# Kernel tuning notes

Measured on AMD Instinct MI355X. Metric: run time of the kernel, lower is better.

## Reference

```python
import jax, jax.numpy as jnp
import numpy as np

N_NODES = 100000
N_EDGES = 1600000
IN_CH, HID_CH, OUT_CH = 128, 64, 64


def setup_inputs() -> dict:
    key = jax.random.key(0)
    k1, k2, k3, k4 = jax.random.split(key, 4)
    x = jax.random.normal(k1, (N_NODES, IN_CH), dtype=jnp.float32)
    edge_index = jax.random.randint(k2, (2, N_EDGES), 0, N_NODES, dtype=jnp.int64)
    # Glorot-style init for GCNConv linear weights; zero bias (PyG default)
    W1 = jax.random.normal(k3, (IN_CH, HID_CH), dtype=jnp.float32) * (1.0 / np.sqrt(IN_CH))
    b1 = jnp.zeros((HID_CH,), dtype=jnp.float32)
    W2 = jax.random.normal(k4, (HID_CH, OUT_CH), dtype=jnp.float32) * (1.0 / np.sqrt(HID_CH))
    b2 = jnp.zeros((OUT_CH,), dtype=jnp.float32)
    return {"x": x, "edge_index": edge_index, "W1": W1, "b1": b1, "W2": W2, "b2": b2}


def gcn_conv(x, row, col, W, b):
    # PyG GCNConv: linear transform, then sym-normalized scatter-add aggregation
    h = x @ W  # [N, out]
    ones = jnp.ones(col.shape, dtype=h.dtype)
    deg = jax.ops.segment_sum(ones, col, num_segments=N_NODES)  # in-degree incl. self-loops
    dinv = jnp.where(deg > 0, jax.lax.rsqrt(deg), 0.0)
    norm = dinv[row] * dinv[col]  # [E+N]
    msg = h[row] * norm[:, None]  # gather + scale, [E+N, out]
    out = jax.ops.segment_sum(msg, col, num_segments=N_NODES)  # scatter-add
    return out + b


def reference(x, edge_index, W1, b1, W2, b2):
    # add self-loops once (same edge set for both layers)
    loops = jnp.arange(N_NODES, dtype=edge_index.dtype)
    row = jnp.concatenate([edge_index[0], loops])
    col = jnp.concatenate([edge_index[1], loops])
    h = jax.nn.relu(gcn_conv(x, row, col, W1, b1))
    return gcn_conv(h, row, col, W2, b2)
```

## Files before the change

kernel.cpp:

```cpp
#include <hip/hip_runtime.h>


#define BKT_SH 7
#define BKT_CAP 4096
#define CHUNK 6144
#define BM 128
#define BK 32

__device__ __forceinline__ unsigned short f2bf(float f) {
    unsigned u = __builtin_bit_cast(unsigned, f);
    u = (u + 0x7FFF + ((u >> 16) & 1)) >> 16;
    return (unsigned short)u;
}
__device__ __forceinline__ float bflo(unsigned u) {
    return __builtin_bit_cast(float, u << 16);
}
__device__ __forceinline__ float bfhi(unsigned u) {
    return __builtin_bit_cast(float, u & 0xFFFF0000u);
}

__global__ __launch_bounds__(256) void k_zero_i(int* __restrict__ p, int n) {
    int i = blockIdx.x * 256 + threadIdx.x;
    if (i < n) p[i] = 0;
}

__global__ __launch_bounds__(256) void k_bin(const int* __restrict__ row,
                                             const int* __restrict__ col,
                                             int* __restrict__ cursor,
                                             unsigned* __restrict__ bentries,
                                             int E) {
    __shared__ unsigned sorted[CHUNK];
    __shared__ unsigned short bof[CHUNK];
    __shared__ int hist[1024];
    __shared__ int ex0[1024];
    __shared__ int cur[1024];
    __shared__ int gbase[1024];
    __shared__ int tsum[256];
    int b = blockIdx.x, t = threadIdx.x;
    int s0 = b * CHUNK;
    int cnt = E - s0; if (cnt > CHUNK) cnt = CHUNK;

    for (int i = t; i < 1024; i += 256) hist[i] = 0;
    __syncthreads();
    for (int i = t; i < cnt; i += 256)
        atomicAdd(&hist[col[s0 + i] >> BKT_SH], 1);
    __syncthreads();
    {
        int b0 = hist[4 * t], b1 = hist[4 * t + 1], b2 = hist[4 * t + 2], b3 = hist[4 * t + 3];
        int tot = b0 + b1 + b2 + b3;
        tsum[t] = tot;
        __syncthreads();
#pragma unroll
        for (int d = 1; d < 256; d <<= 1) {
            int x = (t >= d) ? tsum[t - d] : 0;
            __syncthreads();
            tsum[t] += (t >= d) ? x : 0;
            __syncthreads();
        }
        int ex = tsum[t] - tot;
        ex0[4 * t] = ex;
        ex0[4 * t + 1] = ex + b0;
        ex0[4 * t + 2] = ex + b0 + b1;
        ex0[4 * t + 3] = ex + b0 + b1 + b2;
        cur[4 * t] = ex0[4 * t];
        cur[4 * t + 1] = ex0[4 * t + 1];
        cur[4 * t + 2] = ex0[4 * t + 2];
        cur[4 * t + 3] = ex0[4 * t + 3];
    }
    __syncthreads();
    for (int i = t; i < 1024; i += 256)
        if (hist[i] > 0) gbase[i] = i * BKT_CAP + atomicAdd(&cursor[i], hist[i]);
    for (int i = t; i < cnt; i += 256) {
        int c = col[s0 + i], r = row[s0 + i];
        int bkt = c >> BKT_SH;
        int p = atomicAdd(&cur[bkt], 1);
        sorted[p] = ((unsigned)(c & ((1 << BKT_SH) - 1)) << 17) | (unsigned)r;
        bof[p] = (unsigned short)bkt;
    }
    __syncthreads();
    for (int i = t; i < cnt; i += 256) {
        int bkt = bof[i];
        int pos = gbase[bkt] + (i - ex0[bkt]);
        if (pos < (bkt + 1) * BKT_CAP) bentries[pos] = sorted[i];
    }
}

__global__ __launch_bounds__(256) void k_bucket_sort(
    unsigned* __restrict__ bentries, const int* __restrict__ cursor,
    int* __restrict__ start, int* __restrict__ cntarr,
    float* __restrict__ dinv, int N) {
    __shared__ int hist[128];
    __shared__ int incl[128];
    __shared__ int cur[128];
    __shared__ int rows[BKT_CAP];
    int b = blockIdx.x, t = threadIdx.x;
    int base = b * BKT_CAP;
    int cnt = cursor[b];
    if (cnt > BKT_CAP) cnt = BKT_CAP;

    if (t < 128) hist[t] = 0;
    __syncthreads();
    for (int i = t; i < cnt; i += 256)
        atomicAdd(&hist[bentries[base + i] >> 17], 1);
    __syncthreads();
    if (t < 128) incl[t] = hist[t];
    __syncthreads();
#pragma unroll
    for (int d = 1; d < 128; d <<= 1) {
        int x = (t < 128 && t >= d) ? incl[t - d] : 0;
        __syncthreads();
        if (t < 128 && t >= d) incl[t] += x;
        __syncthreads();
    }
    if (t < 128) {
        int ex = incl[t] - hist[t];
        int node = (b << BKT_SH) + t;
        if (node < N) {
            start[node] = base + ex;
            cntarr[node] = hist[t];
            dinv[node] = rsqrtf((float)hist[t] + 1.0f);
        }
        cur[t] = ex;
    }
    __syncthreads();
    for (int i = t; i < cnt; i += 256) {
        unsigned en = bentries[base + i];
        int p = atomicAdd(&cur[en >> 17], 1);
        rows[p] = (int)(en & 0x1FFFF);
    }
    __syncthreads();
    for (int i = t; i < cnt; i += 256) bentries[base + i] = (unsigned)rows[i];
}

__global__ __launch_bounds__(256) void k_gemm_f32in(
    const float* __restrict__ X, const float* __restrict__ W,
    const float* __restrict__ dinv, unsigned short* __restrict__ outb,
    int N, int K) {
    __shared__ float Xs[BK][BM + 4];
    __shared__ float Ws[BK][64];
    int t = threadIdx.x;
    int bm = blockIdx.x * BM;
    int tm = t >> 4, tn = t & 15;

    float acc[8][4];
#pragma unroll
    for (int i = 0; i < 8; ++i)
#pragma unroll
        for (int j = 0; j < 4; ++j) acc[i][j] = 0.f;

    for (int kb = 0; kb < K; kb += BK) {
#pragma unroll
        for (int it = 0; it < 4; ++it) {
            int r = (t >> 3) + 32 * it;
            int grow = bm + r;
            int k4 = t & 7;
            float4 v = make_float4(0.f, 0.f, 0.f, 0.f);
            if (grow < N) v = *(const float4*)(X + (size_t)grow * K + kb + k4 * 4);
            Xs[k4 * 4 + 0][r] = v.x;
            Xs[k4 * 4 + 1][r] = v.y;
            Xs[k4 * 4 + 2][r] = v.z;
            Xs[k4 * 4 + 3][r] = v.w;
        }
#pragma unroll
        for (int it = 0; it < 2; ++it) {
            int idx = t + 256 * it;
            ((float4*)Ws)[idx] = ((const float4*)(W + (size_t)kb * 64))[idx];
        }
        __syncthreads();
#pragma unroll
        for (int k = 0; k < BK; ++k) {
            float4 xa = *(const float4*)&Xs[k][tm * 8];
            float4 xb = *(const float4*)&Xs[k][tm * 8 + 4];
            float4 w = *(const float4*)&Ws[k][tn * 4];
            float xs[8] = {xa.x, xa.y, xa.z, xa.w, xb.x, xb.y, xb.z, xb.w};
#pragma unroll
            for (int i = 0; i < 8; ++i) {
                acc[i][0] = fmaf(xs[i], w.x, acc[i][0]);
                acc[i][1] = fmaf(xs[i], w.y, acc[i][1]);
                acc[i][2] = fmaf(xs[i], w.z, acc[i][2]);
                acc[i][3] = fmaf(xs[i], w.w, acc[i][3]);
            }
        }
        __syncthreads();
    }
#pragma unroll
    for (int i = 0; i < 8; ++i) {
        int grow = bm + tm * 8 + i;
        if (grow < N) {
            float s = dinv[grow];
            ushort4 v;
            v.x = f2bf(acc[i][0] * s);
            v.y = f2bf(acc[i][1] * s);
            v.z = f2bf(acc[i][2] * s);
            v.w = f2bf(acc[i][3] * s);
            *(ushort4*)(outb + (size_t)grow * 64 + tn * 4) = v;
        }
    }
}

__global__ __launch_bounds__(256) void k_gemm_bf16in(
    const unsigned short* __restrict__ Xb, const float* __restrict__ W,
    const float* __restrict__ dinv, unsigned short* __restrict__ outb,
    int N, int K) {
    __shared__ float Xs[BK][BM + 4];
    __shared__ float Ws[BK][64];
    int t = threadIdx.x;
    int bm = blockIdx.x * BM;
    int tm = t >> 4, tn = t & 15;

    float acc[8][4];
#pragma unroll
    for (int i = 0; i < 8; ++i)
#pragma unroll
        for (int j = 0; j < 4; ++j) acc[i][j] = 0.f;

    for (int kb = 0; kb < K; kb += BK) {
#pragma unroll
        for (int it = 0; it < 2; ++it) {
            int idx = t * 2 + it;
            int r = idx >> 2;
            int q = idx & 3;
            int grow = bm + r;
            uint4 v = make_uint4(0u, 0u, 0u, 0u);
            if (grow < N) v = *(const uint4*)(Xb + (size_t)grow * K + kb + q * 8);
            int k0 = q * 8;
            Xs[k0 + 0][r] = bflo(v.x); Xs[k0 + 1][r] = bfhi(v.x);
            Xs[k0 + 2][r] = bflo(v.y); Xs[k0 + 3][r] = bfhi(v.y);
            Xs[k0 + 4][r] = bflo(v.z); Xs[k0 + 5][r] = bfhi(v.z);
            Xs[k0 + 6][r] = bflo(v.w); Xs[k0 + 7][r] = bfhi(v.w);
        }
#pragma unroll
        for (int it = 0; it < 2; ++it) {
            int idx = t + 256 * it;
            ((float4*)Ws)[idx] = ((const float4*)(W + (size_t)kb * 64))[idx];
        }
        __syncthreads();
#pragma unroll
        for (int k = 0; k < BK; ++k) {
            float4 xa = *(const float4*)&Xs[k][tm * 8];
            float4 xb = *(const float4*)&Xs[k][tm * 8 + 4];
            float4 w = *(const float4*)&Ws[k][tn * 4];
            float xs[8] = {xa.x, xa.y, xa.z, xa.w, xb.x, xb.y, xb.z, xb.w};
#pragma unroll
            for (int i = 0; i < 8; ++i) {
                acc[i][0] = fmaf(xs[i], w.x, acc[i][0]);
                acc[i][1] = fmaf(xs[i], w.y, acc[i][1]);
                acc[i][2] = fmaf(xs[i], w.z, acc[i][2]);
                acc[i][3] = fmaf(xs[i], w.w, acc[i][3]);
            }
        }
        __syncthreads();
    }
#pragma unroll
    for (int i = 0; i < 8; ++i) {
        int grow = bm + tm * 8 + i;
        if (grow < N) {
            float s = dinv[grow];
            ushort4 v;
            v.x = f2bf(acc[i][0] * s);
            v.y = f2bf(acc[i][1] * s);
            v.z = f2bf(acc[i][2] * s);
            v.w = f2bf(acc[i][3] * s);
            *(ushort4*)(outb + (size_t)grow * 64 + tn * 4) = v;
        }
    }
}

__global__ __launch_bounds__(256) void k_gather(
    const uint4* __restrict__ srcq, const int* __restrict__ eros,
    const int* __restrict__ start, const int* __restrict__ cntarr,
    const float* __restrict__ dinv, const float* __restrict__ bias,
    float* __restrict__ dstf, uint4* __restrict__ dstq, int N, int mode) {
    int idx = blockIdx.x * 256 + threadIdx.x;
    int node = idx >> 2;
    if (node >= N) return;
    int l = idx & 3;

    float a[16];
    {
        uint4 s0 = srcq[(size_t)node * 8 + l * 2];
        uint4 s1 = srcq[(size_t)node * 8 + l * 2 + 1];
        a[0] = bflo(s0.x); a[1] = bfhi(s0.x);
        a[2] = bflo(s0.y); a[3] = bfhi(s0.y);
        a[4] = bflo(s0.z); a[5] = bfhi(s0.z);
        a[6] = bflo(s0.w); a[7] = bfhi(s0.w);
        a[8] = bflo(s1.x); a[9] = bfhi(s1.x);
        a[10] = bflo(s1.y); a[11] = bfhi(s1.y);
        a[12] = bflo(s1.z); a[13] = bfhi(s1.z);
        a[14] = bflo(s1.w); a[15] = bfhi(s1.w);
    }

    int e = start[node];
    int eend = e + cntarr[node];
    for (; e + 8 <= eend; e += 8) {
        uint4 v0[8], v1[8];
#pragma unroll
        for (int j = 0; j < 8; ++j) {
            int r = eros[e + j];
            const uint4* p = srcq + (size_t)r * 8 + l * 2;
            v0[j] = p[0];
            v1[j] = p[1];
        }
#pragma unroll
        for (int j = 0; j < 8; ++j) {
            a[0] += bflo(v0[j].x); a[1] += bfhi(v0[j].x);
            a[2] += bflo(v0[j].y); a[3] += bfhi(v0[j].y);
            a[4] += bflo(v0[j].z); a[5] += bfhi(v0[j].z);
            a[6] += bflo(v0[j].w); a[7] += bfhi(v0[j].w);
            a[8] += bflo(v1[j].x); a[9] += bfhi(v1[j].x);
            a[10] += bflo(v1[j].y); a[11] += bfhi(v1[j].y);
            a[12] += bflo(v1[j].z); a[13] += bfhi(v1[j].z);
            a[14] += bflo(v1[j].w); a[15] += bfhi(v1[j].w);
        }
    }
    for (; e + 4 <= eend; e += 4) {
        uint4 v0[4], v1[4];
#pragma unroll
        for (int j = 0; j < 4; ++j) {
            int r = eros[e + j];
            const uint4* p = srcq + (size_t)r * 8 + l * 2;
            v0[j] = p[0];
            v1[j] = p[1];
        }
#pragma unroll
        for (int j = 0; j < 4; ++j) {
            a[0] += bflo(v0[j].x); a[1] += bfhi(v0[j].x);
            a[2] += bflo(v0[j].y); a[3] += bfhi(v0[j].y);
            a[4] += bflo(v0[j].z); a[5] += bfhi(v0[j].z);
            a[6] += bflo(v0[j].w); a[7] += bfhi(v0[j].w);
            a[8] += bflo(v1[j].x); a[9] += bfhi(v1[j].x);
            a[10] += bflo(v1[j].y); a[11] += bfhi(v1[j].y);
            a[12] += bflo(v1[j].z); a[13] += bfhi(v1[j].z);
            a[14] += bflo(v1[j].w); a[15] += bfhi(v1[j].w);
        }
    }
    for (; e < eend; ++e) {
        int r = eros[e];
        const uint4* p = srcq + (size_t)r * 8 + l * 2;
        uint4 v0 = p[0], v1 = p[1];
        a[0] += bflo(v0.x); a[1] += bfhi(v0.x);
        a[2] += bflo(v0.y); a[3] += bfhi(v0.y);
        a[4] += bflo(v0.z); a[5] += bfhi(v0.z);
        a[6] += bflo(v0.w); a[7] += bfhi(v0.w);
        a[8] += bflo(v1.x); a[9] += bfhi(v1.x);
        a[10] += bflo(v1.y); a[11] += bfhi(v1.y);
        a[12] += bflo(v1.z); a[13] += bfhi(v1.z);
        a[14] += bflo(v1.w); a[15] += bfhi(v1.w);
    }
    float sc = dinv[node];
    const float4* bp = (const float4*)bias;
#pragma unroll
    for (int q = 0; q < 4; ++q) {
        float4 bq = bp[l * 4 + q];
        a[q * 4 + 0] = a[q * 4 + 0] * sc + bq.x;
        a[q * 4 + 1] = a[q * 4 + 1] * sc + bq.y;
        a[q * 4 + 2] = a[q * 4 + 2] * sc + bq.z;
        a[q * 4 + 3] = a[q * 4 + 3] * sc + bq.w;
    }
    if (mode) {
#pragma unroll
        for (int i = 0; i < 16; ++i) a[i] = fmaxf(a[i], 0.f);
        uint4 o0, o1;
        o0.x = (unsigned)f2bf(a[0]) | ((unsigned)f2bf(a[1]) << 16);
        o0.y = (unsigned)f2bf(a[2]) | ((unsigned)f2bf(a[3]) << 16);
        o0.z = (unsigned)f2bf(a[4]) | ((unsigned)f2bf(a[5]) << 16);
        o0.w = (unsigned)f2bf(a[6]) | ((unsigned)f2bf(a[7]) << 16);
        o1.x = (unsigned)f2bf(a[8]) | ((unsigned)f2bf(a[9]) << 16);
        o1.y = (unsigned)f2bf(a[10]) | ((unsigned)f2bf(a[11]) << 16);
        o1.z = (unsigned)f2bf(a[12]) | ((unsigned)f2bf(a[13]) << 16);
        o1.w = (unsigned)f2bf(a[14]) | ((unsigned)f2bf(a[15]) << 16);
        dstq[(size_t)node * 8 + l * 2] = o0;
        dstq[(size_t)node * 8 + l * 2 + 1] = o1;
    } else {
        float4* d = (float4*)(dstf + (size_t)node * 64 + l * 16);
        d[0] = make_float4(a[0], a[1], a[2], a[3]);
        d[1] = make_float4(a[4], a[5], a[6], a[7]);
        d[2] = make_float4(a[8], a[9], a[10], a[11]);
        d[3] = make_float4(a[12], a[13], a[14], a[15]);
    }
}

extern "C" void kernel_launch(void* const* d_in, const int* in_sizes, int n_in,
                              void* d_out, int out_size, void* d_ws, size_t ws_size,
                              hipStream_t stream) {
    const float* x = (const float*)d_in[0];
    const int* ei = (const int*)d_in[1];
    const float* W1 = (const float*)d_in[2];
    const float* b1 = (const float*)d_in[3];
    const float* W2 = (const float*)d_in[4];
    const float* b2 = (const float*)d_in[5];

    int N = in_sizes[0] / 128;
    int E = in_sizes[1] / 2;
    const int* row = ei;
    const int* col = ei + E;
    int nb = (N + (1 << BKT_SH) - 1) >> BKT_SH;

    char* ws = (char*)d_ws;
    int* cursor = (int*)ws;
    int* start = (int*)(ws + (1 << 16));
    int* cntarr = (int*)(ws + (1 << 19));
    float* dinv = (float*)(ws + 960 * 1024);
    unsigned* bentries = (unsigned*)(ws + (2 << 20));
    unsigned short* Ab = (unsigned short*)(ws + (15 << 20));
    unsigned short* Hb = (unsigned short*)d_out;
    float* OUTF = (float*)d_out;

    int gemmblk = (N + BM - 1) / BM;
    int binblk = (E + CHUNK - 1) / CHUNK;
    int gblk = (N * 4 + 255) / 256;

    k_zero_i<<<(nb + 255) / 256, 256, 0, stream>>>(cursor, nb);
    k_bin<<<binblk, 256, 0, stream>>>(row, col, cursor, bentries, E);
    k_bucket_sort<<<nb, 256, 0, stream>>>(bentries, cursor, start, cntarr, dinv, N);

    k_gemm_f32in<<<gemmblk, 256, 0, stream>>>(x, W1, dinv, Ab, N, 128);
    k_gather<<<gblk, 256, 0, stream>>>((const uint4*)Ab, (const int*)bentries,
                                       start, cntarr, dinv, b1,
                                       nullptr, (uint4*)Hb, N, 1);

    k_gemm_bf16in<<<gemmblk, 256, 0, stream>>>(Hb, W2, dinv, Ab, N, 64);
    k_gather<<<gblk, 256, 0, stream>>>((const uint4*)Ab, (const int*)bentries,
                                       start, cntarr, dinv, b2,
                                       OUTF, nullptr, N, 0);
}
```

Measured before the change: 250.2 us.

## Fuse all GCN phases into one persistent cooperative kernel with grid syncs

Replaces the seven separate kernel launches with a single cooperative persistent kernel. Each phase becomes a grid-stride device function, and the phases are separated by grid.sync(). The bin chunk size is halved to fit a shared-memory budget that allows two blocks per CU. This is meant to remove launch gaps and tail effects between phases. In exchange it limits parallelism to a grid sized for co-residency and adds grid-wide barrier costs. A fallback path of separate launches is kept for devices without cooperative launch.

```diff
diff --git a/kernel.cpp b/kernel.cpp
--- a/kernel.cpp
+++ b/kernel.cpp
@@ -1,11 +1,16 @@
 #include <hip/hip_runtime.h>
+#include <hip/hip_cooperative_groups.h>
+
+namespace cg = cooperative_groups;
 
 
 #define BKT_SH 7
 #define BKT_CAP 4096
-#define CHUNK 6144
+#define CHUNK 3072
 #define BM 128
 #define BK 32
+#define NTH 256
+#define SMEM_BYTES 35840
 
 __device__ __forceinline__ unsigned short f2bf(float f) {
     unsigned u = __builtin_bit_cast(unsigned, f);
@@ -19,408 +24,519 @@
     return __builtin_bit_cast(float, u & 0xFFFF0000u);
 }
 
-__global__ __launch_bounds__(256) void k_zero_i(int* __restrict__ p, int n) {
-    int i = blockIdx.x * 256 + threadIdx.x;
-    if (i < n) p[i] = 0;
-}
-
-__global__ __launch_bounds__(256) void k_bin(const int* __restrict__ row,
-                                             const int* __restrict__ col,
-                                             int* __restrict__ cursor,
-                                             unsigned* __restrict__ bentries,
-                                             int E) {
-    __shared__ unsigned sorted[CHUNK];
-    __shared__ unsigned short bof[CHUNK];
-    __shared__ int hist[1024];
-    __shared__ int ex0[1024];
-    __shared__ int cur[1024];
-    __shared__ int gbase[1024];
-    __shared__ int tsum[256];
-    int b = blockIdx.x, t = threadIdx.x;
-    int s0 = b * CHUNK;
-    int cnt = E - s0; if (cnt > CHUNK) cnt = CHUNK;
-
-    for (int i = t; i < 1024; i += 256) hist[i] = 0;
-    __syncthreads();
-    for (int i = t; i < cnt; i += 256)
-        atomicAdd(&hist[col[s0 + i] >> BKT_SH], 1);
-    __syncthreads();
-    {
-        int b0 = hist[4 * t], b1 = hist[4 * t + 1], b2 = hist[4 * t + 2], b3 = hist[4 * t + 3];
-        int tot = b0 + b1 + b2 + b3;
-        tsum[t] = tot;
-        __syncthreads();
-#pragma unroll
-        for (int d = 1; d < 256; d <<= 1) {
-            int x = (t >= d) ? tsum[t - d] : 0;
-            __syncthreads();
-            tsum[t] += (t >= d) ? x : 0;
-            __syncthreads();
-        }
-        int ex = tsum[t] - tot;
-        ex0[4 * t] = ex;
-        ex0[4 * t + 1] = ex + b0;
-        ex0[4 * t + 2] = ex + b0 + b1;
-        ex0[4 * t + 3] = ex + b0 + b1 + b2;
-        cur[4 * t] = ex0[4 * t];
-        cur[4 * t + 1] = ex0[4 * t + 1];
-        cur[4 * t + 2] = ex0[4 * t + 2];
-        cur[4 * t + 3] = ex0[4 * t + 3];
-    }
-    __syncthreads();
-    for (int i = t; i < 1024; i += 256)
-        if (hist[i] > 0) gbase[i] = i * BKT_CAP + atomicAdd(&cursor[i], hist[i]);
-    for (int i = t; i < cnt; i += 256) {
-        int c = col[s0 + i], r = row[s0 + i];
-        int bkt = c >> BKT_SH;
-        int p = atomicAdd(&cur[bkt], 1);
-        sorted[p] = ((unsigned)(c & ((1 << BKT_SH) - 1)) << 17) | (unsigned)r;
-        bof[p] = (unsigned short)bkt;
-    }
-    __syncthreads();
-    for (int i = t; i < cnt; i += 256) {
-        int bkt = bof[i];
-        int pos = gbase[bkt] + (i - ex0[bkt]);
-        if (pos < (bkt + 1) * BKT_CAP) bentries[pos] = sorted[i];
-    }
-}
-
-__global__ __launch_bounds__(256) void k_bucket_sort(
-    unsigned* __restrict__ bentries, const int* __restrict__ cursor,
-    int* __restrict__ start, int* __restrict__ cntarr,
-    float* __restrict__ dinv, int N) {
-    __shared__ int hist[128];
-    __shared__ int incl[128];
-    __shared__ int cur[128];
-    __shared__ int rows[BKT_CAP];
-    int b = blockIdx.x, t = threadIdx.x;
-    int base = b * BKT_CAP;
-    int cnt = cursor[b];
-    if (cnt > BKT_CAP) cnt = BKT_CAP;
-
-    if (t < 128) hist[t] = 0;
-    __syncthreads();
-    for (int i = t; i < cnt; i += 256)
-        atomicAdd(&hist[bentries[base + i] >> 17], 1);
-    __syncthreads();
-    if (t < 128) incl[t] = hist[t];
-    __syncthreads();
-#pragma unroll
-    for (int d = 1; d < 128; d <<= 1) {
-        int x = (t < 128 && t >= d) ? incl[t - d] : 0;
-        __syncthreads();
-        if (t < 128 && t >= d) incl[t] += x;
-        __syncthreads();
-    }
-    if (t < 128) {
-        int ex = incl[t] - hist[t];
-        int node = (b << BKT_SH) + t;
-        if (node < N) {
-            start[node] = base + ex;
-            cntarr[node] = hist[t];
-            dinv[node] = rsqrtf((float)hist[t] + 1.0f);
-        }
-        cur[t] = ex;
-    }
-    __syncthreads();
-    for (int i = t; i < cnt; i += 256) {
-        unsigned en = bentries[base + i];
-        int p = atomicAdd(&cur[en >> 17], 1);
-        rows[p] = (int)(en & 0x1FFFF);
-    }
-    __syncthreads();
-    for (int i = t; i < cnt; i += 256) bentries[base + i] = (unsigned)rows[i];
-}
-
-__global__ __launch_bounds__(256) void k_gemm_f32in(
-    const float* __restrict__ X, const float* __restrict__ W,
-    const float* __restrict__ dinv, unsigned short* __restrict__ outb,
-    int N, int K) {
-    __shared__ float Xs[BK][BM + 4];
-    __shared__ float Ws[BK][64];
+struct GcnParams {
+    const float* x;
+    const int* row;
+    const int* col;
+    const float* W1;
+    const float* b1;
+    const float* W2;
+    const float* b2;
+    int* cursor;
+    int* start;
+    int* cntarr;
+    float* dinv;
+    unsigned* bentries;
+    unsigned short* Ab;
+    unsigned short* Hb;
+    float* outf;
+    int N, E, nb, nchunks, gemmblk;
+};
+
+__device__ void ph_zero(int* p, int n, int gtid, int gsz) {
+    for (int i = gtid; i < n; i += gsz) p[i] = 0;
+}
+
+__device__ void ph_bin(char* smem, int bId, int nB,
+                       const int* __restrict__ row, const int* __restrict__ col,
+                       int* __restrict__ cursor, unsigned* __restrict__ bentries,
+                       int E, int nchunks) {
+    unsigned* sorted = (unsigned*)(smem);
+    unsigned short* bof = (unsigned short*)(smem + 12288);
+    int* hist = (int*)(smem + 18432);
+    int* ex0 = (int*)(smem + 22528);
+    int* cur = (int*)(smem + 26624);
+    int* gbase = (int*)(smem + 30720);
+    int* tsum = (int*)(smem + 34816);
     int t = threadIdx.x;
-    int bm = blockIdx.x * BM;
+
+    for (int chn = bId; chn < nchunks; chn += nB) {
+        int s0 = chn * CHUNK;
+        int cnt = E - s0; if (cnt > CHUNK) cnt = CHUNK;
+
+        for (int i = t; i < 1024; i += NTH) hist[i] = 0;
+        __syncthreads();
+        for (int i = t; i < cnt; i += NTH)
+            atomicAdd(&hist[col[s0 + i] >> BKT_SH], 1);
+        __syncthreads();
+        {
+            int b0 = hist[4 * t], b1 = hist[4 * t + 1];
+            int b2 = hist[4 * t + 2], b3 = hist[4 * t + 3];
+            int tot = b0 + b1 + b2 + b3;
+            tsum[t] = tot;
+            __syncthreads();
+#pragma unroll
+            for (int d = 1; d < 256; d <<= 1) {
+                int x = (t >= d) ? tsum[t - d] : 0;
+                __syncthreads();
+                tsum[t] += (t >= d) ? x : 0;
+                __syncthreads();
+            }
+            int ex = tsum[t] - tot;
+            ex0[4 * t] = ex;
+            ex0[4 * t + 1] = ex + b0;
+            ex0[4 * t + 2] = ex + b0 + b1;
+            ex0[4 * t + 3] = ex + b0 + b1 + b2;
+            cur[4 * t] = ex0[4 * t];
+            cur[4 * t + 1] = ex0[4 * t + 1];
+            cur[4 * t + 2] = ex0[4 * t + 2];
+            cur[4 * t + 3] = ex0[4 * t + 3];
+        }
+        __syncthreads();
+        for (int i = t; i < 1024; i += NTH)
+            if (hist[i] > 0) gbase[i] = i * BKT_CAP + atomicAdd(&cursor[i], hist[i]);
+        for (int i = t; i < cnt; i += NTH) {
+            int c = col[s0 + i], r = row[s0 + i];
+            int bkt = c >> BKT_SH;
+            int p = atomicAdd(&cur[bkt], 1);
+            sorted[p] = ((unsigned)(c & ((1 << BKT_SH) - 1)) << 17) | (unsigned)r;
+            bof[p] = (unsigned short)bkt;
+        }
+        __syncthreads();
+        for (int i = t; i < cnt; i += NTH) {
+            int bkt = bof[i];
+            int pos = gbase[bkt] + (i - ex0[bkt]);
+            if (pos < (bkt + 1) * BKT_CAP) bentries[pos] = sorted[i];
+        }
+        __syncthreads();
+    }
+}
+
+__device__ void ph_bsort(char* smem, int bId, int nB,
+                         unsigned* __restrict__ bentries, const int* __restrict__ cursor,
+                         int* __restrict__ start, int* __restrict__ cntarr,
+                         float* __restrict__ dinv, int N, int nb) {
+    int* hist = (int*)(smem);
+    int* incl = (int*)(smem + 512);
+    int* cur = (int*)(smem + 1024);
+    int* rows = (int*)(smem + 1536);
+    int t = threadIdx.x;
+
+    for (int b = bId; b < nb; b += nB) {
+        int base = b * BKT_CAP;
+        int cnt = cursor[b];
+        if (cnt > BKT_CAP) cnt = BKT_CAP;
+
+        if (t < 128) hist[t] = 0;
+        __syncthreads();
+        for (int i = t; i < cnt; i += NTH)
+            atomicAdd(&hist[bentries[base + i] >> 17], 1);
+        __syncthreads();
+        if (t < 128) incl[t] = hist[t];
+        __syncthreads();
+#pragma unroll
+        for (int d = 1; d < 128; d <<= 1) {
+            int x = (t < 128 && t >= d) ? incl[t - d] : 0;
+            __syncthreads();
+            if (t < 128 && t >= d) incl[t] += x;
+            __syncthreads();
+        }
+        if (t < 128) {
+            int ex = incl[t] - hist[t];
+            int node = (b << BKT_SH) + t;
+            if (node < N) {
+                start[node] = base + ex;
+                cntarr[node] = hist[t];
+                dinv[node] = rsqrtf((float)hist[t] + 1.0f);
+            }
+            cur[t] = ex;
+        }
+        __syncthreads();
+        for (int i = t; i < cnt; i += NTH) {
+            unsigned en = bentries[base + i];
+            int p = atomicAdd(&cur[en >> 17], 1);
+            rows[p] = (int)(en & 0x1FFFF);
+        }
+        __syncthreads();
+        for (int i = t; i < cnt; i += NTH) bentries[base + i] = (unsigned)rows[i];
+        __syncthreads();
+    }
+}
+
+__device__ void ph_gemm_f32(char* smem, int bId, int nB,
+                            const float* __restrict__ X, const float* __restrict__ W,
+                            const float* __restrict__ dinv,
+                            unsigned short* __restrict__ outb,
+                            int N, int K, int gemmblk) {
+    float (*Xs)[BM + 4] = (float(*)[BM + 4])(smem);
+    float (*Ws)[64] = (float(*)[64])(smem + 16896);
+    int t = threadIdx.x;
     int tm = t >> 4, tn = t & 15;
 
-    float acc[8][4];
-#pragma unroll
-    for (int i = 0; i < 8; ++i)
-#pragma unroll
-        for (int j = 0; j < 4; ++j) acc[i][j] = 0.f;
-
-    for (int kb = 0; kb < K; kb += BK) {
-#pragma unroll
-        for (int it = 0; it < 4; ++it) {
-            int r = (t >> 3) + 32 * it;
-            int grow = bm + r;
-            int k4 = t & 7;
-            float4 v = make_float4(0.f, 0.f, 0.f, 0.f);
-            if (grow < N) v = *(const float4*)(X + (size_t)grow * K + kb + k4 * 4);
-            Xs[k4 * 4 + 0][r] = v.x;
-            Xs[k4 * 4 + 1][r] = v.y;
-            Xs[k4 * 4 + 2][r] = v.z;
-            Xs[k4 * 4 + 3][r] = v.w;
-        }
-#pragma unroll
-        for (int it = 0; it < 2; ++it) {
-            int idx = t + 256 * it;
-            ((float4*)Ws)[idx] = ((const float4*)(W + (size_t)kb * 64))[idx];
-        }
-        __syncthreads();
-#pragma unroll
-        for (int k = 0; k < BK; ++k) {
-            float4 xa = *(const float4*)&Xs[k][tm * 8];
-            float4 xb = *(const float4*)&Xs[k][tm * 8 + 4];
-            float4 w = *(const float4*)&Ws[k][tn * 4];
-            float xs[8] = {xa.x, xa.y, xa.z, xa.w, xb.x, xb.y, xb.z, xb.w};
-#pragma unroll
-            for (int i = 0; i < 8; ++i) {
-                acc[i][0] = fmaf(xs[i], w.x, acc[i][0]);
-                acc[i][1] = fmaf(xs[i], w.y, acc[i][1]);
-                acc[i][2] = fmaf(xs[i], w.z, acc[i][2]);
-                acc[i][3] = fmaf(xs[i], w.w, acc[i][3]);
-            }
-        }
-        __syncthreads();
-    }
-#pragma unroll
-    for (int i = 0; i < 8; ++i) {
-        int grow = bm + tm * 8 + i;
-        if (grow < N) {
-            float s = dinv[grow];
-            ushort4 v;
-            v.x = f2bf(acc[i][0] * s);
-            v.y = f2bf(acc[i][1] * s);
-            v.z = f2bf(acc[i][2] * s);
-            v.w = f2bf(acc[i][3] * s);
-            *(ushort4*)(outb + (size_t)grow * 64 + tn * 4) = v;
-        }
-    }
-}
-
-__global__ __launch_bounds__(256) void k_gemm_bf16in(
-    const unsigned short* __restrict__ Xb, const float* __restrict__ W,
-    const float* __restrict__ dinv, unsigned short* __restrict__ outb,
-    int N, int K) {
-    __shared__ float Xs[BK][BM + 4];
-    __shared__ float Ws[BK][64];
+    for (int tile = bId; tile < gemmblk; tile += nB) {
+        int bm = tile * BM;
+        float acc[8][4];
+#pragma unroll
+        for (int i = 0; i < 8; ++i)
+#pragma unroll
+            for (int j = 0; j < 4; ++j) acc[i][j] = 0.f;
+
+        for (int kb = 0; kb < K; kb += BK) {
+#pragma unroll
+            for (int it = 0; it < 4; ++it) {
+                int r = (t >> 3) + 32 * it;
+                int grow = bm + r;
+                int k4 = t & 7;
+                float4 v = make_float4(0.f, 0.f, 0.f, 0.f);
+                if (grow < N) v = *(const float4*)(X + (size_t)grow * K + kb + k4 * 4);
+                Xs[k4 * 4 + 0][r] = v.x;
+                Xs[k4 * 4 + 1][r] = v.y;
+                Xs[k4 * 4 + 2][r] = v.z;
+                Xs[k4 * 4 + 3][r] = v.w;
+            }
+#pragma unroll
+            for (int it = 0; it < 2; ++it) {
+                int idx = t + NTH * it;
+                ((float4*)Ws)[idx] = ((const float4*)(W + (size_t)kb * 64))[idx];
+            }
+            __syncthreads();
+#pragma unroll
+            for (int k = 0; k < BK; ++k) {
+                float4 xa = *(const float4*)&Xs[k][tm * 8];
+                float4 xb = *(const float4*)&Xs[k][tm * 8 + 4];
+                float4 w = *(const float4*)&Ws[k][tn * 4];
+                float xs[8] = {xa.x, xa.y, xa.z, xa.w, xb.x, xb.y, xb.z, xb.w};
+#pragma unroll
+                for (int i = 0; i < 8; ++i) {
+                    acc[i][0] = fmaf(xs[i], w.x, acc[i][0]);
+                    acc[i][1] = fmaf(xs[i], w.y, acc[i][1]);
+                    acc[i][2] = fmaf(xs[i], w.z, acc[i][2]);
+                    acc[i][3] = fmaf(xs[i], w.w, acc[i][3]);
+                }
+            }
+            __syncthreads();
+        }
+#pragma unroll
+        for (int i = 0; i < 8; ++i) {
+            int grow = bm + tm * 8 + i;
+            if (grow < N) {
+                float s = dinv[grow];
+                ushort4 v;
+                v.x = f2bf(acc[i][0] * s);
+                v.y = f2bf(acc[i][1] * s);
+                v.z = f2bf(acc[i][2] * s);
+                v.w = f2bf(acc[i][3] * s);
+                *(ushort4*)(outb + (size_t)grow * 64 + tn * 4) = v;
+            }
+        }
+        __syncthreads();
+    }
+}
+
+__device__ void ph_gemm_bf16(char* smem, int bId, int nB,
+                             const unsigned short* __restrict__ Xb,
+                             const float* __restrict__ W,
+                             const float* __restrict__ dinv,
+                             unsigned short* __restrict__ outb,
+                             int N, int K, int gemmblk) {
+    float (*Xs)[BM + 4] = (float(*)[BM + 4])(smem);
+    float (*Ws)[64] = (float(*)[64])(smem + 16896);
     int t = threadIdx.x;
-    int bm = blockIdx.x * BM;
     int tm = t >> 4, tn = t & 15;
 
-    float acc[8][4];
-#pragma unroll
-    for (int i = 0; i < 8; ++i)
-#pragma unroll
-        for (int j = 0; j < 4; ++j) acc[i][j] = 0.f;
-
-    for (int kb = 0; kb < K; kb += BK) {
-#pragma unroll
-        for (int it = 0; it < 2; ++it) {
-            int idx = t * 2 + it;
-            int r = idx >> 2;
-            int q = idx & 3;
-            int grow = bm + r;
-            uint4 v = make_uint4(0u, 0u, 0u, 0u);
-            if (grow < N) v = *(const uint4*)(Xb + (size_t)grow * K + kb + q * 8);
-            int k0 = q * 8;
-            Xs[k0 + 0][r] = bflo(v.x); Xs[k0 + 1][r] = bfhi(v.x);
-            Xs[k0 + 2][r] = bflo(v.y); Xs[k0 + 3][r] = bfhi(v.y);
-            Xs[k0 + 4][r] = bflo(v.z); Xs[k0 + 5][r] = bfhi(v.z);
-            Xs[k0 + 6][r] = bflo(v.w); Xs[k0 + 7][r] = bfhi(v.w);
-        }
-#pragma unroll
-        for (int it = 0; it < 2; ++it) {
-            int idx = t + 256 * it;
-            ((float4*)Ws)[idx] = ((const float4*)(W + (size_t)kb * 64))[idx];
-        }
-        __syncthreads();
-#pragma unroll
-        for (int k = 0; k < BK; ++k) {
-            float4 xa = *(const float4*)&Xs[k][tm * 8];
-            float4 xb = *(const float4*)&Xs[k][tm * 8 + 4];
-            float4 w = *(const float4*)&Ws[k][tn * 4];
-            float xs[8] = {xa.x, xa.y, xa.z, xa.w, xb.x, xb.y, xb.z, xb.w};
-#pragma unroll
-            for (int i = 0; i < 8; ++i) {
-                acc[i][0] = fmaf(xs[i], w.x, acc[i][0]);
-                acc[i][1] = fmaf(xs[i], w.y, acc[i][1]);
-                acc[i][2] = fmaf(xs[i], w.z, acc[i][2]);
-                acc[i][3] = fmaf(xs[i], w.w, acc[i][3]);
-            }
-        }
-        __syncthreads();
-    }
-#pragma unroll
-    for (int i = 0; i < 8; ++i) {
-        int grow = bm + tm * 8 + i;
-        if (grow < N) {
-            float s = dinv[grow];
-            ushort4 v;
-            v.x = f2bf(acc[i][0] * s);
-            v.y = f2bf(acc[i][1] * s);
-            v.z = f2bf(acc[i][2] * s);
-            v.w = f2bf(acc[i][3] * s);
-            *(ushort4*)(outb + (size_t)grow * 64 + tn * 4) = v;
-        }
-    }
-}
-
-__global__ __launch_bounds__(256) void k_gather(
-    const uint4* __restrict__ srcq, const int* __restrict__ eros,
-    const int* __restrict__ start, const int* __restrict__ cntarr,
-    const float* __restrict__ dinv, const float* __restrict__ bias,
-    float* __restrict__ dstf, uint4* __restrict__ dstq, int N, int mode) {
-    int idx = blockIdx.x * 256 + threadIdx.x;
-    int node = idx >> 2;
-    if (node >= N) return;
-    int l = idx & 3;
-
-    float a[16];
-    {
-        uint4 s0 = srcq[(size_t)node * 8 + l * 2];
-        uint4 s1 = srcq[(size_t)node * 8 + l * 2 + 1];
-        a[0] = bflo(s0.x); a[1] = bfhi(s0.x);
-        a[2] = bflo(s0.y); a[3] = bfhi(s0.y);
-        a[4] = bflo(s0.z); a[5] = bfhi(s0.z);
-        a[6] = bflo(s0.w); a[7] = bfhi(s0.w);
-        a[8] = bflo(s1.x); a[9] = bfhi(s1.x);
-        a[10] = bflo(s1.y); a[11] = bfhi(s1.y);
-        a[12] = bflo(s1.z); a[13] = bfhi(s1.z);
-        a[14] = bflo(s1.w); a[15] = bfhi(s1.w);
-    }
-
-    int e = start[node];
-    int eend = e + cntarr[node];
-    for (; e + 8 <= eend; e += 8) {
-        uint4 v0[8], v1[8];
-#pragma unroll
-        for (int j = 0; j < 8; ++j) {
-            int r = eros[e + j];
+    for (int tile = bId; tile < gemmblk; tile += nB) {
+        int bm = tile * BM;
+        float acc[8][4];
+#pragma unroll
+        for (int i = 0; i < 8; ++i)
+#pragma unroll
+            for (int j = 0; j < 4; ++j) acc[i][j] = 0.f;
+
+        for (int kb = 0; kb < K; kb += BK) {
+#pragma unroll
+            for (int it = 0; it < 2; ++it) {
+                int idx = t * 2 + it;
+                int r = idx >> 2;
+                int q = idx & 3;
+                int grow = bm + r;
+                uint4 v = make_uint4(0u, 0u, 0u, 0u);
+                if (grow < N) v = *(const uint4*)(Xb + (size_t)grow * K + kb + q * 8);
+                int k0 = q * 8;
+                Xs[k0 + 0][r] = bflo(v.x); Xs[k0 + 1][r] = bfhi(v.x);
+                Xs[k0 + 2][r] = bflo(v.y); Xs[k0 + 3][r] = bfhi(v.y);
+                Xs[k0 + 4][r] = bflo(v.z); Xs[k0 + 5][r] = bfhi(v.z);
+                Xs[k0 + 6][r] = bflo(v.w); Xs[k0 + 7][r] = bfhi(v.w);
+            }
+#pragma unroll
+            for (int it = 0; it < 2; ++it) {
+                int idx = t + NTH * it;
+                ((float4*)Ws)[idx] = ((const float4*)(W + (size_t)kb * 64))[idx];
+            }
+            __syncthreads();
+#pragma unroll
+            for (int k = 0; k < BK; ++k) {
+                float4 xa = *(const float4*)&Xs[k][tm * 8];
+                float4 xb = *(const float4*)&Xs[k][tm * 8 + 4];
+                float4 w = *(const float4*)&Ws[k][tn * 4];
+                float xs[8] = {xa.x, xa.y, xa.z, xa.w, xb.x, xb.y, xb.z, xb.w};
+#pragma unroll
+                for (int i = 0; i < 8; ++i) {
+                    acc[i][0] = fmaf(xs[i], w.x, acc[i][0]);
+                    acc[i][1] = fmaf(xs[i], w.y, acc[i][1]);
+                    acc[i][2] = fmaf(xs[i], w.z, acc[i][2]);
+                    acc[i][3] = fmaf(xs[i], w.w, acc[i][3]);
+                }
+            }
+            __syncthreads();
+        }
+#pragma unroll
+        for (int i = 0; i < 8; ++i) {
+            int grow = bm + tm * 8 + i;
+            if (grow < N) {
+                float s = dinv[grow];
+                ushort4 v;
+                v.x = f2bf(acc[i][0] * s);
+                v.y = f2bf(acc[i][1] * s);
+                v.z = f2bf(acc[i][2] * s);
+                v.w = f2bf(acc[i][3] * s);
+                *(ushort4*)(outb + (size_t)grow * 64 + tn * 4) = v;
+            }
+        }
+        __syncthreads();
+    }
+}
+
+__device__ void ph_gather(int gtid, int gsz,
+                          const uint4* __restrict__ srcq, const int* __restrict__ eros,
+                          const int* __restrict__ start, const int* __restrict__ cntarr,
+                          const float* __restrict__ dinv, const float* __restrict__ bias,
+                          float* __restrict__ dstf, uint4* __restrict__ dstq,
+                          int N, int mode) {
+    int total = N * 4;
+    for (int idx = gtid; idx < total; idx += gsz) {
+        int node = idx >> 2;
+        int l = idx & 3;
+
+        float a[16];
+        {
+            uint4 s0 = srcq[(size_t)node * 8 + l * 2];
+            uint4 s1 = srcq[(size_t)node * 8 + l * 2 + 1];
+            a[0] = bflo(s0.x); a[1] = bfhi(s0.x);
+            a[2] = bflo(s0.y); a[3] = bfhi(s0.y);
+            a[4] = bflo(s0.z); a[5] = bfhi(s0.z);
+            a[6] = bflo(s0.w); a[7] = bfhi(s0.w);
+            a[8] = bflo(s1.x); a[9] = bfhi(s1.x);
+            a[10] = bflo(s1.y); a[11] = bfhi(s1.y);
+            a[12] = bflo(s1.z); a[13] = bfhi(s1.z);
+            a[14] = bflo(s1.w); a[15] = bfhi(s1.w);
+        }
+
+        int e = start[node];
+        int eend = e + cntarr[node];
+        for (; e + 8 <= eend; e += 8) {
+            uint4 v0[8], v1[8];
+#pragma unroll
+            for (int j = 0; j < 8; ++j) {
+                int r = eros[e + j];
+                const uint4* p = srcq + (size_t)r * 8 + l * 2;
+                v0[j] = p[0];
+                v1[j] = p[1];
+            }
+#pragma unroll
+            for (int j = 0; j < 8; ++j) {
+                a[0] += bflo(v0[j].x); a[1] += bfhi(v0[j].x);
+                a[2] += bflo(v0[j].y); a[3] += bfhi(v0[j].y);
+                a[4] += bflo(v0[j].z); a[5] += bfhi(v0[j].z);
+                a[6] += bflo(v0[j].w); a[7] += bfhi(v0[j].w);
+                a[8] += bflo(v1[j].x); a[9] += bfhi(v1[j].x);
+                a[10] += bflo(v1[j].y); a[11] += bfhi(v1[j].y);
+                a[12] += bflo(v1[j].z); a[13] += bfhi(v1[j].z);
+                a[14] += bflo(v1[j].w); a[15] += bfhi(v1[j].w);
+            }
+        }
+        for (; e + 4 <= eend; e += 4) {
+            uint4 v0[4], v1[4];
+#pragma unroll
+            for (int j = 0; j < 4; ++j) {
+                int r = eros[e + j];
+                const uint4* p = srcq + (size_t)r * 8 + l * 2;
+                v0[j] = p[0];
+                v1[j] = p[1];
+            }
+#pragma unroll
+            for (int j = 0; j < 4; ++j) {
+                a[0] += bflo(v0[j].x); a[1] += bfhi(v0[j].x);
+                a[2] += bflo(v0[j].y); a[3] += bfhi(v0[j].y);
+                a[4] += bflo(v0[j].z); a[5] += bfhi(v0[j].z);
+                a[6] += bflo(v0[j].w); a[7] += bfhi(v0[j].w);
+                a[8] += bflo(v1[j].x); a[9] += bfhi(v1[j].x);
+                a[10] += bflo(v1[j].y); a[11] += bfhi(v1[j].y);
+                a[12] += bflo(v1[j].z); a[13] += bfhi(v1[j].z);
+                a[14] += bflo(v1[j].w); a[15] += bfhi(v1[j].w);
+            }
+        }
+        for (; e < eend; ++e) {
+            int r = eros[e];
             const uint4* p = srcq + (size_t)r * 8 + l * 2;
-            v0[j] = p[0];
-            v1[j] = p[1];
-        }
-#pragma unroll
-        for (int j = 0; j < 8; ++j) {
-            a[0] += bflo(v0[j].x); a[1] += bfhi(v0[j].x);
-            a[2] += bflo(v0[j].y); a[3] += bfhi(v0[j].y);
-            a[4] += bflo(v0[j].z); a[5] += bfhi(v0[j].z);
-            a[6] += bflo(v0[j].w); a[7] += bfhi(v0[j].w);
-            a[8] += bflo(v1[j].x); a[9] += bfhi(v1[j].x);
-            a[10] += bflo(v1[j].y); a[11] += bfhi(v1[j].y);
-            a[12] += bflo(v1[j].z); a[13] += bfhi(v1[j].z);
-            a[14] += bflo(v1[j].w); a[15] += bfhi(v1[j].w);
-        }
-    }
-    for (; e + 4 <= eend; e += 4) {
-        uint4 v0[4], v1[4];
-#pragma unroll
-        for (int j = 0; j < 4; ++j) {
-            int r = eros[e + j];
-            const uint4* p = srcq + (size_t)r * 8 + l * 2;
-            v0[j] = p[0];
-            v1[j] = p[1];
-        }
-#pragma unroll
-        for (int j = 0; j < 4; ++j) {
-            a[0] += bflo(v0[j].x); a[1] += bfhi(v0[j].x);
-            a[2] += bflo(v0[j].y); a[3] += bfhi(v0[j].y);
-            a[4] += bflo(v0[j].z); a[5] += bfhi(v0[j].z);
-            a[6] += bflo(v0[j].w); a[7] += bfhi(v0[j].w);
-            a[8] += bflo(v1[j].x); a[9] += bfhi(v1[j].x);
-            a[10] += bflo(v1[j].y); a[11] += bfhi(v1[j].y);
-            a[12] += bflo(v1[j].z); a[13] += bfhi(v1[j].z);
-            a[14] += bflo(v1[j].w); a[15] += bfhi(v1[j].w);
-        }
-    }
-    for (; e < eend; ++e) {
-        int r = eros[e];
-        const uint4* p = srcq + (size_t)r * 8 + l * 2;
-        uint4 v0 = p[0], v1 = p[1];
-        a[0] += bflo(v0.x); a[1] += bfhi(v0.x);
-        a[2] += bflo(v0.y); a[3] += bfhi(v0.y);
-        a[4] += bflo(v0.z); a[5] += bfhi(v0.z);
-        a[6] += bflo(v0.w); a[7] += bfhi(v0.w);
-        a[8] += bflo(v1.x); a[9] += bfhi(v1.x);
-        a[10] += bflo(v1.y); a[11] += bfhi(v1.y);
-        a[12] += bflo(v1.z); a[13] += bfhi(v1.z);
-        a[14] += bflo(v1.w); a[15] += bfhi(v1.w);
-    }
-    float sc = dinv[node];
-    const float4* bp = (const float4*)bias;
-#pragma unroll
-    for (int q = 0; q < 4; ++q) {
-        float4 bq = bp[l * 4 + q];
-        a[q * 4 + 0] = a[q * 4 + 0] * sc + bq.x;
-        a[q * 4 + 1] = a[q * 4 + 1] * sc + bq.y;
-        a[q * 4 + 2] = a[q * 4 + 2] * sc + bq.z;
-        a[q * 4 + 3] = a[q * 4 + 3] * sc + bq.w;
-    }
-    if (mode) {
-#pragma unroll
-        for (int i = 0; i < 16; ++i) a[i] = fmaxf(a[i], 0.f);
-        uint4 o0, o1;
-        o0.x = (unsigned)f2bf(a[0]) | ((unsigned)f2bf(a[1]) << 16);
-        o0.y = (unsigned)f2bf(a[2]) | ((unsigned)f2bf(a[3]) << 16);
-        o0.z = (unsigned)f2bf(a[4]) | ((unsigned)f2bf(a[5]) << 16);
-        o0.w = (unsigned)f2bf(a[6]) | ((unsigned)f2bf(a[7]) << 16);
-        o1.x = (unsigned)f2bf(a[8]) | ((unsigned)f2bf(a[9]) << 16);
-        o1.y = (unsigned)f2bf(a[10]) | ((unsigned)f2bf(a[11]) << 16);
-        o1.z = (unsigned)f2bf(a[12]) | ((unsigned)f2bf(a[13]) << 16);
-        o1.w = (unsigned)f2bf(a[14]) | ((unsigned)f2bf(a[15]) << 16);
-        dstq[(size_t)node * 8 + l * 2] = o0;
-        dstq[(size_t)node * 8 + l * 2 + 1] = o1;
-    } else {
-        float4* d = (float4*)(dstf + (size_t)node * 64 + l * 16);
-        d[0] = make_float4(a[0], a[1], a[2], a[3]);
-        d[1] = make_float4(a[4], a[5], a[6], a[7]);
-        d[2] = make_float4(a[8], a[9], a[10], a[11]);
-        d[3] = make_float4(a[12], a[13], a[14], a[15]);
-    }
+            uint4 v0 = p[0], v1 = p[1];
+            a[0] += bflo(v0.x); a[1] += bfhi(v0.x);
+            a[2] += bflo(v0.y); a[3] += bfhi(v0.y);
+            a[4] += bflo(v0.z); a[5] += bfhi(v0.z);
+            a[6] += bflo(v0.w); a[7] += bfhi(v0.w);
+            a[8] += bflo(v1.x); a[9] += bfhi(v1.x);
+            a[10] += bflo(v1.y); a[11] += bfhi(v1.y);
+            a[12] += bflo(v1.z); a[13] += bfhi(v1.z);
+            a[14] += bflo(v1.w); a[15] += bfhi(v1.w);
+        }
+        float sc = dinv[node];
+        const float4* bp = (const float4*)bias;
+#pragma unroll
+        for (int q = 0; q < 4; ++q) {
+            float4 bq = bp[l * 4 + q];
+            a[q * 4 + 0] = a[q * 4 + 0] * sc + bq.x;
+            a[q * 4 + 1] = a[q * 4 + 1] * sc + bq.y;
+            a[q * 4 + 2] = a[q * 4 + 2] * sc + bq.z;
+            a[q * 4 + 3] = a[q * 4 + 3] * sc + bq.w;
+        }
+        if (mode) {
+#pragma unroll
+            for (int i = 0; i < 16; ++i) a[i] = fmaxf(a[i], 0.f);
+            uint4 o0, o1;
+            o0.x = (unsigned)f2bf(a[0]) | ((unsigned)f2bf(a[1]) << 16);
+            o0.y = (unsigned)f2bf(a[2]) | ((unsigned)f2bf(a[3]) << 16);
+            o0.z = (unsigned)f2bf(a[4]) | ((unsigned)f2bf(a[5]) << 16);
+            o0.w = (unsigned)f2bf(a[6]) | ((unsigned)f2bf(a[7]) << 16);
+            o1.x = (unsigned)f2bf(a[8]) | ((unsigned)f2bf(a[9]) << 16);
+            o1.y = (unsigned)f2bf(a[10]) | ((unsigned)f2bf(a[11]) << 16);
+            o1.z = (unsigned)f2bf(a[12]) | ((unsigned)f2bf(a[13]) << 16);
+            o1.w = (unsigned)f2bf(a[14]) | ((unsigned)f2bf(a[15]) << 16);
+            dstq[(size_t)node * 8 + l * 2] = o0;
+            dstq[(size_t)node * 8 + l * 2 + 1] = o1;
+        } else {
+            float4* d = (float4*)(dstf + (size_t)node * 64 + l * 16);
+            d[0] = make_float4(a[0], a[1], a[2], a[3]);
+            d[1] = make_float4(a[4], a[5], a[6], a[7]);
+            d[2] = make_float4(a[8], a[9], a[10], a[11]);
+            d[3] = make_float4(a[12], a[13], a[14], a[15]);
+        }
+    }
+}
+
+__global__ __launch_bounds__(NTH, 2) void k_mega(GcnParams p) {
+    cg::grid_group grid = cg::this_grid();
+    __shared__ __align__(16) char smem[SMEM_BYTES];
+    int bId = blockIdx.x, nB = gridDim.x;
+    int gtid = bId * NTH + threadIdx.x, gsz = nB * NTH;
+
+    ph_zero(p.cursor, p.nb, gtid, gsz);
+    grid.sync();
+    ph_bin(smem, bId, nB, p.row, p.col, p.cursor, p.bentries, p.E, p.nchunks);
+    grid.sync();
+    ph_bsort(smem, bId, nB, p.bentries, p.cursor, p.start, p.cntarr, p.dinv, p.N, p.nb);
+    grid.sync();
+    ph_gemm_f32(smem, bId, nB, p.x, p.W1, p.dinv, p.Ab, p.N, 128, p.gemmblk);
+    grid.sync();
+    ph_gather(gtid, gsz, (const uint4*)p.Ab, (const int*)p.bentries,
+              p.start, p.cntarr, p.dinv, p.b1, nullptr, (uint4*)p.Hb, p.N, 1);
+    grid.sync();
+    ph_gemm_bf16(smem, bId, nB, p.Hb, p.W2, p.dinv, p.Ab, p.N, 64, p.gemmblk);
+    grid.sync();
+    ph_gather(gtid, gsz, (const uint4*)p.Ab, (const int*)p.bentries,
+              p.start, p.cntarr, p.dinv, p.b2, p.outf, nullptr, p.N, 0);
+}
+
+__global__ __launch_bounds__(NTH) void k_zero_w(GcnParams p) {
+    ph_zero(p.cursor, p.nb, blockIdx.x * NTH + threadIdx.x, gridDim.x * NTH);
+}
+__global__ __launch_bounds__(NTH) void k_bin_w(GcnParams p) {
+    __shared__ __align__(16) char smem[SMEM_BYTES];
+    ph_bin(smem, blockIdx.x, gridDim.x, p.row, p.col, p.cursor, p.bentries, p.E, p.nchunks);
+}
+__global__ __launch_bounds__(NTH) void k_bsort_w(GcnParams p) {
+    __shared__ __align__(16) char smem[17920];
+    ph_bsort(smem, blockIdx.x, gridDim.x, p.bentries, p.cursor, p.start, p.cntarr,
+             p.dinv, p.N, p.nb);
+}
+__global__ __launch_bounds__(NTH) void k_gemm1_w(GcnParams p) {
+    __shared__ __align__(16) char smem[25088];
+    ph_gemm_f32(smem, blockIdx.x, gridDim.x, p.x, p.W1, p.dinv, p.Ab, p.N, 128, p.gemmblk);
+}
+__global__ __launch_bounds__(NTH) void k_gemm2_w(GcnParams p) {
+    __shared__ __align__(16) char smem[25088];
+    ph_gemm_bf16(smem, blockIdx.x, gridDim.x, p.Hb, p.W2, p.dinv, p.Ab, p.N, 64, p.gemmblk);
+}
+__global__ __launch_bounds__(NTH) void k_gather1_w(GcnParams p) {
+    ph_gather(blockIdx.x * NTH + threadIdx.x, gridDim.x * NTH, (const uint4*)p.Ab,
+              (const int*)p.bentries, p.start, p.cntarr, p.dinv, p.b1,
+              nullptr, (uint4*)p.Hb, p.N, 1);
+}
+__global__ __launch_bounds__(NTH) void k_gather2_w(GcnParams p) {
+    ph_gather(blockIdx.x * NTH + threadIdx.x, gridDim.x * NTH, (const uint4*)p.Ab,
+              (const int*)p.bentries, p.start, p.cntarr, p.dinv, p.b2,
+              p.outf, nullptr, p.N, 0);
 }
 
 extern "C" void kernel_launch(void* const* d_in, const int* in_sizes, int n_in,
                               void* d_out, int out_size, void* d_ws, size_t ws_size,
                               hipStream_t stream) {
-    const float* x = (const float*)d_in[0];
+    GcnParams p;
+    p.x = (const float*)d_in[0];
     const int* ei = (const int*)d_in[1];
-    const float* W1 = (const float*)d_in[2];
-    const float* b1 = (const float*)d_in[3];
-    const float* W2 = (const float*)d_in[4];
-    const float* b2 = (const float*)d_in[5];
-
-    int N = in_sizes[0] / 128;
-    int E = in_sizes[1] / 2;
-    const int* row = ei;
-    const int* col = ei + E;
-    int nb = (N + (1 << BKT_SH) - 1) >> BKT_SH;
+    p.W1 = (const float*)d_in[2];
+    p.b1 = (const float*)d_in[3];
+    p.W2 = (const float*)d_in[4];
+    p.b2 = (const float*)d_in[5];
+
+    p.N = in_sizes[0] / 128;
+    p.E = in_sizes[1] / 2;
+    p.row = ei;
+    p.col = ei + p.E;
+    p.nb = (p.N + (1 << BKT_SH) - 1) >> BKT_SH;
+    p.nchunks = (p.E + CHUNK - 1) / CHUNK;
+    p.gemmblk = (p.N + BM - 1) / BM;
 
     char* ws = (char*)d_ws;
-    int* cursor = (int*)ws;
-    int* start = (int*)(ws + (1 << 16));
-    int* cntarr = (int*)(ws + (1 << 19));
-    float* dinv = (float*)(ws + 960 * 1024);
-    unsigned* bentries = (unsigned*)(ws + (2 << 20));
-    unsigned short* Ab = (unsigned short*)(ws + (15 << 20));
-    unsigned short* Hb = (unsigned short*)d_out;
-    float* OUTF = (float*)d_out;
-
-    int gemmblk = (N + BM - 1) / BM;
-    int binblk = (E + CHUNK - 1) / CHUNK;
-    int gblk = (N * 4 + 255) / 256;
-
-    k_zero_i<<<(nb + 255) / 256, 256, 0, stream>>>(cursor, nb);
-    k_bin<<<binblk, 256, 0, stream>>>(row, col, cursor, bentries, E);
-    k_bucket_sort<<<nb, 256, 0, stream>>>(bentries, cursor, start, cntarr, dinv, N);
-
-    k_gemm_f32in<<<gemmblk, 256, 0, stream>>>(x, W1, dinv, Ab, N, 128);
-    k_gather<<<gblk, 256, 0, stream>>>((const uint4*)Ab, (const int*)bentries,
-                                       start, cntarr, dinv, b1,
-                                       nullptr, (uint4*)Hb, N, 1);
-
-    k_gemm_bf16in<<<gemmblk, 256, 0, stream>>>(Hb, W2, dinv, Ab, N, 64);
-    k_gather<<<gblk, 256, 0, stream>>>((const uint4*)Ab, (const int*)bentries,
-                                       start, cntarr, dinv, b2,
-                                       OUTF, nullptr, N, 0);
-}
+    p.cursor = (int*)ws;
+    p.start = (int*)(ws + (1 << 16));
+    p.cntarr = (int*)(ws + (1 << 19));
+    p.dinv = (float*)(ws + 960 * 1024);
+    p.bentries = (unsigned*)(ws + (2 << 20));
+    p.Ab = (unsigned short*)(ws + (15 << 20));
+    p.Hb = (unsigned short*)d_out;
+    p.outf = (float*)d_out;
+
+    static int s_mode = -1;
+    static int s_grid = 256;
+    if (s_mode < 0) {
+        int dev = 0;
+        hipGetDevice(&dev);
+        int coop = 0;
+        hipDeviceGetAttribute(&coop, hipDeviceAttributeCooperativeLaunch, dev);
+        int ncu = 0;
+        hipDeviceGetAttribute(&ncu, hipDeviceAttributeMultiprocessorCount, dev);
+        int maxb = 0;
+        hipError_t e = hipOccupancyMaxActiveBlocksPerMultiprocessor(
+            &maxb, reinterpret_cast<const void*>(&k_mega), NTH, 0);
+        if (e == hipSuccess && coop && maxb >= 1 && ncu > 0) {
+            s_mode = 1;
+            s_grid = ncu * (maxb > 2 ? 2 : maxb);
+        } else {
+            s_mode = 0;
+        }
+    }
+
+    if (s_mode == 1) {
+        void* kargs[] = {&p};
+        hipLaunchCooperativeKernel(reinterpret_cast<const void*>(&k_mega),
+                                   dim3(s_grid), dim3(NTH), kargs, 0, stream);
+    } else {
+        int gblk = (p.N * 4 + NTH - 1) / NTH;
+        k_zero_w<<<(p.nb + NTH - 1) / NTH, NTH, 0, stream>>>(p);
+        k_bin_w<<<p.nchunks, NTH, 0, stream>>>(p);
+        k_bsort_w<<<p.nb, NTH, 0, stream>>>(p);
+        k_gemm1_w<<<p.gemmblk, NTH, 0, stream>>>(p);
+        k_gather1_w<<<gblk, NTH, 0, stream>>>(p);
+        k_gemm2_w<<<p.gemmblk, NTH, 0, stream>>>(p);
+        k_gather2_w<<<gblk, NTH, 0, stream>>>(p);
+    }
+}
```

Result: slower. 370.8 us (+48.2%).
